# Optimization experiments

Measured on AMD Instinct MI355X. Metric: run time of the kernel, lower is better.

The kernel has to match this reference:

```python
import jax, jax.numpy as jnp
import numpy as np
from jax import lax

L, D, V, T = 12, 1024, 50277, 1024
F4 = 4 * D


def setup_inputs() -> dict:
    key = jax.random.key(0)
    ks = jax.random.split(key, 20)
    s = 0.02  # weight scale keeps k (exp argument) well-conditioned
    n = lambda k, shape, scale=s: jax.random.normal(k, shape, dtype=jnp.float32) * scale
    u = lambda k, shape: jax.random.uniform(k, shape, dtype=jnp.float32)
    return {
        "tokens": jax.random.randint(ks[0], (T,), 0, V, dtype=jnp.int32),
        "emb": n(ks[1], (V, D), 1.0),
        "ln0_w": jnp.ones((D,), jnp.float32), "ln0_b": jnp.zeros((D,), jnp.float32),
        "ln1_w": jnp.ones((L, D), jnp.float32), "ln1_b": jnp.zeros((L, D), jnp.float32),
        "ln2_w": jnp.ones((L, D), jnp.float32), "ln2_b": jnp.zeros((L, D), jnp.float32),
        "tmk": u(ks[2], (L, D)), "tmv": u(ks[3], (L, D)), "tmr": u(ks[4], (L, D)),
        "tmk_ffn": u(ks[5], (L, D)), "tmr_ffn": u(ks[6], (L, D)),
        "time_first": n(ks[7], (L, D), 0.5),
        "time_decay": -jnp.exp(n(ks[8], (L, D), 0.5)),  # __init__: -exp(raw)
        "att_kw": n(ks[9], (L, D, D)), "att_vw": n(ks[10], (L, D, D)),
        "att_rw": n(ks[11], (L, D, D)), "att_ow": n(ks[12], (L, D, D)),
        "ffn_kw": n(ks[13], (L, D, F4)), "ffn_vw": n(ks[14], (L, F4, D)),
        "ffn_rw": n(ks[15], (L, D, D)),
        "lnout_w": jnp.ones((D,), jnp.float32), "lnout_b": jnp.zeros((D,), jnp.float32),
        "head": n(ks[16], (V, D)),
    }


def _ln(x, w, b):
    mu = jnp.mean(x, -1, keepdims=True)
    var = jnp.var(x, -1, keepdims=True)
    return (x - mu) / jnp.sqrt(var + 1e-5) * w + b


def _shift(x):  # token shift: prepend zero state row (state init is zeros)
    return jnp.concatenate([jnp.zeros_like(x[:1]), x[:-1]], axis=0)


def _wkv(k, v, tf, td):  # k,v: [T,D]; aa/bb/pp scan with running-max exp trick
    init = (jnp.zeros_like(k[0]), jnp.zeros_like(k[0]), jnp.full_like(k[0], -1e30))
    def step(c, kv):
        aa, bb, pp = c
        kt, vt = kv
        ww = tf + kt
        p = jnp.maximum(pp, ww)
        e1 = jnp.exp(pp - p); e2 = jnp.exp(ww - p)
        out = (e1 * aa + e2 * vt) / (e1 * bb + e2)
        ww2 = pp + td
        p2 = jnp.maximum(ww2, kt)
        e1 = jnp.exp(ww2 - p2); e2 = jnp.exp(kt - p2)
        return (e1 * aa + e2 * vt, e1 * bb + e2, p2), out
    _, out = lax.scan(step, init, (k, v))
    return out


def reference(tokens, emb, ln0_w, ln0_b, ln1_w, ln1_b, ln2_w, ln2_b, tmk, tmv, tmr,
              tmk_ffn, tmr_ffn, time_first, time_decay, att_kw, att_vw, att_rw, att_ow,
              ffn_kw, ffn_vw, ffn_rw, lnout_w, lnout_b, head):
    x = _ln(emb[tokens], ln0_w, ln0_b)  # [T,D]; ln0 applied to emb rows as in __init__
    for i in range(L):
        # time-mix (attention) block
        xn = _ln(x, ln1_w[i], ln1_b[i])
        xx = _shift(xn)
        xk = xn * tmk[i] + xx * (1 - tmk[i])
        xv = xn * tmv[i] + xx * (1 - tmv[i])
        xr = xn * tmr[i] + xx * (1 - tmr[i])
        r = jax.nn.sigmoid(xr @ att_rw[i])
        k = xk @ att_kw[i]
        v = xv @ att_vw[i]
        wkv = _wkv(k, v, time_first[i], time_decay[i])
        x = x + (r * wkv) @ att_ow[i]
        # channel-mix (ffn) block
        xn = _ln(x, ln2_w[i], ln2_b[i])
        xx = _shift(xn)
        xk = xn * tmk_ffn[i] + xx * (1 - tmk_ffn[i])
        xr = xn * tmr_ffn[i] + xx * (1 - tmr_ffn[i])
        rf = jax.nn.sigmoid(xr @ ffn_rw[i])
        kf = jnp.square(jax.nn.relu(xk @ ffn_kw[i]))
        x = x + rf * (kf @ ffn_vw[i])
    xo = _ln(x[-1], lnout_w, lnout_b)
    return head @ xo  # logits [V]
```

## Files before the change

### kernel.cpp

```cpp
#include <hip/hip_runtime.h>

#define Tn 1024
#define Dn 1024
#define Ln 12
#define F4n 4096
#define Vn 50277
#define TDn (Tn*Dn)
#define MEG 1048576
#define SEG 16
#define NSEG 64

typedef __attribute__((ext_vector_type(4))) float f4;
typedef __attribute__((ext_vector_type(16))) float f32x16;
typedef __attribute__((ext_vector_type(8))) short short8;
typedef unsigned short u16;
typedef unsigned int u32;
typedef __attribute__((ext_vector_type(4))) u16 us4;

#define ASG __attribute__((address_space(1)))
#define ASL __attribute__((address_space(3)))

__device__ __forceinline__ u16 f2b(float x){
  u32 u = __float_as_uint(x);
  return (u16)((u + 0x7fffu + ((u >> 16) & 1u)) >> 16);
}

__device__ __forceinline__ f4 blockReduce4(f4 v){
  __shared__ f4 s[4];
  int lane = threadIdx.x & 63, w = threadIdx.x >> 6;
#pragma unroll
  for(int o = 32; o; o >>= 1){
    v.x += __shfl_xor(v.x, o);
    v.y += __shfl_xor(v.y, o);
    v.z += __shfl_xor(v.z, o);
    v.w += __shfl_xor(v.w, o);
  }
  if(lane == 0) s[w] = v;
  __syncthreads();
  return s[0] + s[1] + s[2] + s[3];
}

struct ConvArgs {
  const float* s0; const float* s1; const float* s2; const float* s3;
  const float* skw;
  const float* svw;
  const float* srw;
  u16* dst;
};
__global__ __launch_bounds__(256) void conv_k(ConvArgs a){
  __shared__ __align__(16) u16 t[64][68];
  int b = blockIdx.x, tid = threadIdx.x;
  const float* src; u16* dst; int K, N, tk, tn;
  if(b < 1024){
    int m = b >> 8, bt = b & 255;
    src = (m==0)?a.s0:((m==1)?a.s1:((m==2)?a.s2:a.s3));
    dst = a.dst + (size_t)m*MEG; K=1024; N=1024; tk=bt>>4; tn=bt&15;
  } else if(b < 2048){
    int bt = b-1024; src=a.skw; dst=a.dst+(size_t)4*MEG; K=1024; N=4096; tk=bt>>6; tn=bt&63;
  } else if(b < 3072){
    int bt = b-2048; src=a.svw; dst=a.dst+(size_t)8*MEG; K=4096; N=1024; tk=bt>>4; tn=bt&15;
  } else {
    int bt = b-3072; src=a.srw; dst=a.dst+(size_t)12*MEG; K=1024; N=1024; tk=bt>>4; tn=bt&15;
  }
  int rr0 = tid >> 4, c4 = (tid & 15)*4;
#pragma unroll
  for(int p=0;p<4;p++){
    int r = p*16 + rr0;
    f4 v = *(const f4*)(src + (size_t)(tk*64+r)*N + tn*64 + c4);
    us4 h; h[0]=f2b(v.x); h[1]=f2b(v.y); h[2]=f2b(v.z); h[3]=f2b(v.w);
    *(us4*)&t[r][c4] = h;
  }
  __syncthreads();
  int q = tid & 3, n = tid >> 2;
  int k0 = q*16;
  union { short8 v; u16 h[8]; } o0, o1;
#pragma unroll
  for(int j=0;j<8;j++){ o0.h[j]=t[k0+j][n]; o1.h[j]=t[k0+8+j][n]; }
  u16* dp = dst + (size_t)(tn*64+n)*K + tk*64 + k0;
  *(short8*)dp       = o0.v;
  *(short8*)(dp + 8) = o1.v;
}

__global__ __launch_bounds__(256) void embed_ln0_k(
    const int* __restrict__ tok, const float* __restrict__ emb,
    const float* __restrict__ w, const float* __restrict__ b,
    float* __restrict__ x){
  int t = blockIdx.x, tid = threadIdx.x;
  const f4* src = (const f4*)(emb + (size_t)tok[t] * Dn);
  f4 v = src[tid];
  f4 st;
  st.x = v.x+v.y+v.z+v.w;
  st.y = v.x*v.x+v.y*v.y+v.z*v.z+v.w*v.w;
  st.z = 0.f; st.w = 0.f;
  f4 red = blockReduce4(st);
  float mu = red.x * (1.0f/Dn);
  float rs = rsqrtf(red.y * (1.0f/Dn) - mu*mu + 1e-5f);
  f4 wv = ((const f4*)w)[tid], bv = ((const f4*)b)[tid];
  f4 o;
  o.x = (v.x-mu)*rs*wv.x + bv.x;
  o.y = (v.y-mu)*rs*wv.y + bv.y;
  o.z = (v.z-mu)*rs*wv.z + bv.z;
  o.w = (v.w-mu)*rs*wv.w + bv.w;
  ((f4*)(x + (size_t)t*Dn))[tid] = o;
}

__global__ __launch_bounds__(256) void ln_mix_att_k(
    const float* __restrict__ x,
    const float* __restrict__ lw, const float* __restrict__ lb,
    const float* __restrict__ tk, const float* __restrict__ tv, const float* __restrict__ tr,
    u16* __restrict__ xkvr){
  int t = blockIdx.x, tid = threadIdx.x;
  f4 cur = ((const f4*)(x + (size_t)t*Dn))[tid];
  f4 prv; prv.x=0.f; prv.y=0.f; prv.z=0.f; prv.w=0.f;
  if(t > 0) prv = ((const f4*)(x + (size_t)(t-1)*Dn))[tid];
  f4 st;
  st.x = cur.x+cur.y+cur.z+cur.w;
  st.y = cur.x*cur.x+cur.y*cur.y+cur.z*cur.z+cur.w*cur.w;
  st.z = prv.x+prv.y+prv.z+prv.w;
  st.w = prv.x*prv.x+prv.y*prv.y+prv.z*prv.z+prv.w*prv.w;
  f4 red = blockReduce4(st);
  float muc = red.x*(1.f/Dn), rsc = rsqrtf(red.y*(1.f/Dn)-muc*muc+1e-5f);
  float mup = red.z*(1.f/Dn), rsp = rsqrtf(red.w*(1.f/Dn)-mup*mup+1e-5f);
  f4 wv=((const f4*)lw)[tid], bv=((const f4*)lb)[tid];
  f4 kv=((const f4*)tk)[tid], vv=((const f4*)tv)[tid], rv=((const f4*)tr)[tid];
  us4 ok, ov, orr;
  float xn, xp;
#define MIX3(j, cj, pj, wj, bj, kj, vj, rj) \
  xn = (cj - muc)*rsc*wj + bj; \
  xp = (t>0) ? ((pj - mup)*rsp*wj + bj) : 0.f; \
  ok[j]  = f2b(xn*kj + xp*(1.f-kj)); \
  ov[j]  = f2b(xn*vj + xp*(1.f-vj)); \
  orr[j] = f2b(xn*rj + xp*(1.f-rj));
  MIX3(0, cur.x, prv.x, wv.x, bv.x, kv.x, vv.x, rv.x)
  MIX3(1, cur.y, prv.y, wv.y, bv.y, kv.y, vv.y, rv.y)
  MIX3(2, cur.z, prv.z, wv.z, bv.z, kv.z, vv.z, rv.z)
  MIX3(3, cur.w, prv.w, wv.w, bv.w, kv.w, vv.w, rv.w)
#undef MIX3
  size_t o0 = (size_t)t*Dn + tid*4;
  *(us4*)(xkvr + o0)         = ok;
  *(us4*)(xkvr + TDn + o0)   = ov;
  *(us4*)(xkvr + 2*TDn + o0) = orr;
}

__global__ __launch_bounds__(256) void ln_mix_ffn_k(
    const float* __restrict__ x,
    const float* __restrict__ lw, const float* __restrict__ lb,
    const float* __restrict__ tk, const float* __restrict__ tr,
    u16* __restrict__ xkr){
  int t = blockIdx.x, tid = threadIdx.x;
  f4 cur = ((const f4*)(x + (size_t)t*Dn))[tid];
  f4 prv; prv.x=0.f; prv.y=0.f; prv.z=0.f; prv.w=0.f;
  if(t > 0) prv = ((const f4*)(x + (size_t)(t-1)*Dn))[tid];
  f4 st;
  st.x = cur.x+cur.y+cur.z+cur.w;
  st.y = cur.x*cur.x+cur.y*cur.y+cur.z*cur.z+cur.w*cur.w;
  st.z = prv.x+prv.y+prv.z+prv.w;
  st.w = prv.x*prv.x+prv.y*prv.y+prv.z*prv.z+prv.w*prv.w;
  f4 red = blockReduce4(st);
  float muc = red.x*(1.f/Dn), rsc = rsqrtf(red.y*(1.f/Dn)-muc*muc+1e-5f);
  float mup = red.z*(1.f/Dn), rsp = rsqrtf(red.w*(1.f/Dn)-mup*mup+1e-5f);
  f4 wv=((const f4*)lw)[tid], bv=((const f4*)lb)[tid];
  f4 kv=((const f4*)tk)[tid], rv=((const f4*)tr)[tid];
  us4 ok, orr;
  float xn, xp;
#define MIX2(j, cj, pj, wj, bj, kj, rj) \
  xn = (cj - muc)*rsc*wj + bj; \
  xp = (t>0) ? ((pj - mup)*rsp*wj + bj) : 0.f; \
  ok[j]  = f2b(xn*kj + xp*(1.f-kj)); \
  orr[j] = f2b(xn*rj + xp*(1.f-rj));
  MIX2(0, cur.x, prv.x, wv.x, bv.x, kv.x, rv.x)
  MIX2(1, cur.y, prv.y, wv.y, bv.y, kv.y, rv.y)
  MIX2(2, cur.z, prv.z, wv.z, bv.z, kv.z, rv.z)
  MIX2(3, cur.w, prv.w, wv.w, bv.w, kv.w, rv.w)
#undef MIX2
  size_t o0 = (size_t)t*Dn + tid*4;
  *(us4*)(xkr + o0)       = ok;
  *(us4*)(xkr + TDn + o0) = orr;
}

__global__ __launch_bounds__(256) void wkv_seg_k(
    const float* __restrict__ kb, const float* __restrict__ vb,
    const float* __restrict__ tdp,
    float* __restrict__ sega, float* __restrict__ segb, float* __restrict__ segp){
  int ch = blockIdx.x*256 + threadIdx.x;
  int g = blockIdx.y;
  int t0 = g*SEG;
  float td = tdp[ch];
  float kk[SEG], vv[SEG];
#pragma unroll
  for(int j=0;j<SEG;j++){
    kk[j] = kb[(size_t)(t0+j)*Dn + ch];
    vv[j] = vb[(size_t)(t0+j)*Dn + ch];
  }
  float aa=0.f, bb=0.f, pp=-1e30f;
#pragma unroll
  for(int j=0;j<SEG;j++){
    float ww2 = pp + td;
    float p2 = fmaxf(ww2, kk[j]);
    float e1 = __expf(ww2-p2), e2 = __expf(kk[j]-p2);
    aa = e1*aa + e2*vv[j]; bb = e1*bb + e2; pp = p2;
  }
  size_t o = (size_t)g*Dn + ch;
  sega[o] = aa; segb[o] = bb; segp[o] = pp;
}

__global__ __launch_bounds__(256) void wkv_scan_k(
    const float* __restrict__ sega, const float* __restrict__ segb, const float* __restrict__ segp,
    const float* __restrict__ tdp,
    float* __restrict__ prea, float* __restrict__ preb, float* __restrict__ prep){
  int ch = blockIdx.x*256 + threadIdx.x;
  float Std = tdp[ch] * (float)SEG;
  float a=0.f, b=0.f, p=-1e30f;
  for(int g=0; g<NSEG; g++){
    size_t o = (size_t)g*Dn + ch;
    prea[o]=a; preb[o]=b; prep[o]=p;
    float ag=sega[o], bg=segb[o], qg=segp[o];
    float psh = p + Std;
    float pn = fmaxf(psh, qg);
    float eo = __expf(psh-pn), en = __expf(qg-pn);
    a = eo*a + en*ag; b = eo*b + en*bg; p = pn;
  }
}

__global__ __launch_bounds__(256) void wkv_out_k(
    const float* __restrict__ kb, const float* __restrict__ vb, const float* __restrict__ rb,
    const float* __restrict__ tfp, const float* __restrict__ tdp,
    const float* __restrict__ prea, const float* __restrict__ preb, const float* __restrict__ prep,
    u16* __restrict__ att_in){
  int ch = blockIdx.x*256 + threadIdx.x;
  int g = blockIdx.y;
  int t0 = g*SEG;
  float tf = tfp[ch], td = tdp[ch];
  size_t so = (size_t)g*Dn + ch;
  float aa = prea[so], bb = preb[so], pp = prep[so];
  float kk[SEG], vv[SEG], rr[SEG];
#pragma unroll
  for(int j=0;j<SEG;j++){
    kk[j]=kb[(size_t)(t0+j)*Dn+ch];
    vv[j]=vb[(size_t)(t0+j)*Dn+ch];
    rr[j]=rb[(size_t)(t0+j)*Dn+ch];
  }
#pragma unroll
  for(int j=0;j<SEG;j++){
    float kt=kk[j], vt=vv[j];
    float ww = tf + kt;
    float p = fmaxf(pp, ww);
    float e1 = __expf(pp-p), e2 = __expf(ww-p);
    float out = __fdividef(e1*aa+e2*vt, e1*bb+e2);
    float sig = __fdividef(1.f, 1.f+__expf(-rr[j]));
    att_in[(size_t)(t0+j)*Dn+ch] = f2b(sig*out);
    float ww2 = pp+td;
    float p2 = fmaxf(ww2,kt);
    e1 = __expf(ww2-p2); e2 = __expf(kt-p2);
    aa = e1*aa+e2*vt; bb = e1*bb+e2; pp = p2;
  }
}

template<int EPI, int KSTEP>
__global__ __launch_bounds__(128) void gemm_k(
    const u16* __restrict__ A, size_t ldA, size_t strideA,
    const u16* __restrict__ Bt, size_t ldB, size_t strideB,
    int K, int N,
    float* __restrict__ Cf, size_t strideC, u16* __restrict__ Cb,
    const float* __restrict__ aux){
  extern __shared__ __align__(16) u16 ldsd[];
  constexpr int RPC = 512/KSTEP;
  constexpr int LPR = 64/RPC;
  constexpr int NQ  = 32/RPC;
  constexpr int NS  = KSTEP/32;
  const int tid = threadIdx.x;
  const int l = tid & 63, w = tid >> 6;
  const int z = blockIdx.z;
  const int row0 = blockIdx.y*64, col0 = blockIdx.x*64;

  const u16* bA = A  + (size_t)z*strideA + (size_t)row0*ldA;
  const u16* bB = Bt + (size_t)z*strideB + (size_t)col0*ldB;

  int offA[NQ], offB[NQ], ldso[NQ];
#pragma unroll
  for(int q=0;q<NQ;q++){
    int ch = q*2 + w;
    int r  = ch*RPC + l/LPR;
    int phys = (l%LPR)*16;
    int kk = ((phys ^ ((r&15)<<4)) >> 1);
    offA[q] = r*(int)ldA + kk;
    offB[q] = r*(int)ldB + kk;
    ldso[q] = ch*512;
  }
  int foff[2][NS];
#pragma unroll
  for(int i=0;i<2;i++){
    int row = i*32 + (l&31);
#pragma unroll
    for(int s=0;s<NS;s++){
      int c = w*KSTEP + s*32 + ((l>>5)*16);
      foff[i][s] = row*KSTEP + ((c ^ ((row&15)<<4)) >> 1);
    }
  }

  f32x16 acc[2][2];
#pragma unroll
  for(int i=0;i<2;i++)
#pragma unroll
    for(int j=0;j<2;j++)
#pragma unroll
      for(int e=0;e<16;e++) acc[i][j][e] = 0.f;

  u16* ldsA0 = ldsd;
  u16* ldsB0 = ldsd + 64*KSTEP;
  u16* ldsA1 = ldsd + 2*64*KSTEP;
  u16* ldsB1 = ldsd + 3*64*KSTEP;

#define STAGE(LA, LB) do{ \
  _Pragma("unroll") \
  for(int q=0;q<NQ;q++){ \
    __builtin_amdgcn_global_load_lds((ASG const void*)(const void*)(bA + offA[q]), (ASL void*)(void*)((LA) + ldso[q]), 16, 0, 0); \
    __builtin_amdgcn_global_load_lds((ASG const void*)(const void*)(bB + offB[q]), (ASL void*)(void*)((LB) + ldso[q]), 16, 0, 0); \
  } \
  bA += KSTEP; bB += KSTEP; }while(0)

  const int nss = K / KSTEP;
  STAGE(ldsA0, ldsB0);
  __syncthreads();
  int buf = 0;
  for(int ss=0; ss<nss; ss++){
    if(ss+1 < nss){
      if(buf) STAGE(ldsA0, ldsB0); else STAGE(ldsA1, ldsB1);
    }
    const u16* La = buf ? ldsA1 : ldsA0;
    const u16* Lb = buf ? ldsB1 : ldsB0;
#pragma unroll
    for(int s=0;s<NS;s++){
      short8 a0 = *(const short8*)(La + foff[0][s]);
      short8 a1 = *(const short8*)(La + foff[1][s]);
      short8 b0 = *(const short8*)(Lb + foff[0][s]);
      short8 b1 = *(const short8*)(Lb + foff[1][s]);
      acc[0][0] = __builtin_amdgcn_mfma_f32_32x32x16_bf16(a0, b0, acc[0][0], 0, 0, 0);
      acc[0][1] = __builtin_amdgcn_mfma_f32_32x32x16_bf16(a0, b1, acc[0][1], 0, 0, 0);
      acc[1][0] = __builtin_amdgcn_mfma_f32_32x32x16_bf16(a1, b0, acc[1][0], 0, 0, 0);
      acc[1][1] = __builtin_amdgcn_mfma_f32_32x32x16_bf16(a1, b1, acc[1][1], 0, 0, 0);
    }
    __syncthreads();
    buf ^= 1;
  }
#undef STAGE

  float* red = (float*)ldsd;
  if(w == 1){
#pragma unroll
    for(int i=0;i<2;i++)
#pragma unroll
      for(int j=0;j<2;j++)
#pragma unroll
        for(int reg=0;reg<16;reg++){
          int rr_ = (reg&3) + 8*(reg>>2) + 4*(l>>5);
          red[(size_t)(i*32 + rr_)*64 + j*32 + (l&31)] = acc[i][j][reg];
        }
  }
  __syncthreads();
  if(w == 0){
#pragma unroll
    for(int i=0;i<2;i++)
#pragma unroll
      for(int j=0;j<2;j++)
#pragma unroll
        for(int reg=0;reg<16;reg++){
          int rr_ = (reg&3) + 8*(reg>>2) + 4*(l>>5);
          float v = acc[i][j][reg] + red[(size_t)(i*32 + rr_)*64 + j*32 + (l&31)];
          int grow = row0 + i*32 + rr_;
          int gcol = col0 + j*32 + (l&31);
          size_t idx = (size_t)grow*N + gcol;
          if constexpr(EPI==0){ Cf[(size_t)z*strideC + idx] = v; }
          else if constexpr(EPI==1){ float t_ = v>0.f ? v : 0.f; Cb[idx] = f2b(t_*t_); }
          else if constexpr(EPI==2){ Cf[idx] += v; }
          else { float s_ = __fdividef(1.f, 1.f+__expf(-aux[idx])); Cf[idx] += s_*v; }
        }
  }
}

__global__ __launch_bounds__(256) void lnout_k(
    const float* __restrict__ x, const float* __restrict__ w, const float* __restrict__ b,
    float* __restrict__ xo){
  int tid = threadIdx.x;
  f4 v = ((const f4*)(x + (size_t)(Tn-1)*Dn))[tid];
  f4 st;
  st.x = v.x+v.y+v.z+v.w;
  st.y = v.x*v.x+v.y*v.y+v.z*v.z+v.w*v.w;
  st.z = 0.f; st.w = 0.f;
  f4 red = blockReduce4(st);
  float mu = red.x*(1.f/Dn);
  float rs = rsqrtf(red.y*(1.f/Dn) - mu*mu + 1e-5f);
  f4 wv = ((const f4*)w)[tid], bv = ((const f4*)b)[tid];
  f4 o;
  o.x = (v.x-mu)*rs*wv.x + bv.x;
  o.y = (v.y-mu)*rs*wv.y + bv.y;
  o.z = (v.z-mu)*rs*wv.z + bv.z;
  o.w = (v.w-mu)*rs*wv.w + bv.w;
  ((f4*)xo)[tid] = o;
}

__global__ __launch_bounds__(256) void head_k(
    const float* __restrict__ head, const float* __restrict__ xo, float* __restrict__ out){
  __shared__ f4 sxo[256];
  int tid = threadIdx.x;
  sxo[tid] = ((const f4*)xo)[tid];
  __syncthreads();
  int w = tid >> 6, lane = tid & 63;
  int row = blockIdx.x*4 + w;
  if(row < Vn){
    const f4* hr = (const f4*)(head + (size_t)row*Dn);
    float s = 0.f;
#pragma unroll
    for(int i=0;i<4;i++){
      f4 h = hr[i*64 + lane];
      f4 xv = sxo[i*64 + lane];
      s += h.x*xv.x + h.y*xv.y + h.z*xv.z + h.w*xv.w;
    }
#pragma unroll
    for(int o=32;o;o>>=1) s += __shfl_xor(s, o);
    if(lane == 0) out[row] = s;
  }
}

extern "C" void kernel_launch(void* const* d_in, const int* in_sizes, int n_in,
                              void* d_out, int out_size, void* d_ws, size_t ws_size,
                              hipStream_t stream) {
  (void)in_sizes; (void)n_in; (void)out_size; (void)ws_size;
  const int*   tokens   = (const int*)  d_in[0];
  const float* emb      = (const float*)d_in[1];
  const float* ln0_w    = (const float*)d_in[2];
  const float* ln0_b    = (const float*)d_in[3];
  const float* ln1_w    = (const float*)d_in[4];
  const float* ln1_b    = (const float*)d_in[5];
  const float* ln2_w    = (const float*)d_in[6];
  const float* ln2_b    = (const float*)d_in[7];
  const float* tmk      = (const float*)d_in[8];
  const float* tmv      = (const float*)d_in[9];
  const float* tmr      = (const float*)d_in[10];
  const float* tmk_ffn  = (const float*)d_in[11];
  const float* tmr_ffn  = (const float*)d_in[12];
  const float* tfirst   = (const float*)d_in[13];
  const float* tdecay   = (const float*)d_in[14];
  const float* att_kw   = (const float*)d_in[15];
  const float* att_vw   = (const float*)d_in[16];
  const float* att_rw   = (const float*)d_in[17];
  const float* att_ow   = (const float*)d_in[18];
  const float* ffn_kw   = (const float*)d_in[19];
  const float* ffn_vw   = (const float*)d_in[20];
  const float* ffn_rw   = (const float*)d_in[21];
  const float* lnoutw   = (const float*)d_in[22];
  const float* lnoutb   = (const float*)d_in[23];
  const float* headw    = (const float*)d_in[24];
  float* logits = (float*)d_out;

  char* wsb = (char*)d_ws;
  size_t off = 0;
  auto carve = [&](size_t bytes)->void*{
    void* p = wsb + off;
    off += (bytes + 255) & ~(size_t)255;
    return p;
  };
  float* x      = (float*)carve((size_t)TDn*4);
  u16*   xkvr   = (u16*)  carve((size_t)3*TDn*2);
  float* kvr    = (float*)carve((size_t)3*TDn*4);
  u16*   att_in = (u16*)  carve((size_t)TDn*2);
  u16*   xkr    = (u16*)  carve((size_t)2*TDn*2);
  u16*   kf     = (u16*)  carve((size_t)Tn*F4n*2);
  float* rf     = (float*)carve((size_t)TDn*4);
  float* xo     = (float*)carve((size_t)Dn*4);
  u16*   wbt    = (u16*)  carve((size_t)13*MEG*2);
  float* sega   = (float*)carve((size_t)NSEG*Dn*4);
  float* segb   = (float*)carve((size_t)NSEG*Dn*4);
  float* segp   = (float*)carve((size_t)NSEG*Dn*4);
  float* prea   = (float*)carve((size_t)NSEG*Dn*4);
  float* preb   = (float*)carve((size_t)NSEG*Dn*4);
  float* prep   = (float*)carve((size_t)NSEG*Dn*4);

  embed_ln0_k<<<Tn, 256, 0, stream>>>(tokens, emb, ln0_w, ln0_b, x);

  for(int i=0;i<Ln;i++){
    size_t dd = (size_t)i*Dn*Dn;
    ConvArgs ca;
    ca.s0 = att_kw+dd; ca.s1 = att_vw+dd; ca.s2 = att_rw+dd; ca.s3 = att_ow+dd;
    ca.skw = ffn_kw+(size_t)i*Dn*F4n; ca.svw = ffn_vw+(size_t)i*F4n*Dn; ca.srw = ffn_rw+dd;
    ca.dst = wbt;
    conv_k<<<3328, 256, 0, stream>>>(ca);

    ln_mix_att_k<<<Tn, 256, 0, stream>>>(x, ln1_w+i*Dn, ln1_b+i*Dn,
                                         tmk+i*Dn, tmv+i*Dn, tmr+i*Dn, xkvr);
    gemm_k<0,128><<<dim3(16,16,3), 128, 65536, stream>>>(
        xkvr, Dn, (size_t)TDn, wbt, Dn, (size_t)MEG, Dn, Dn,
        kvr, (size_t)TDn, nullptr, nullptr);
    wkv_seg_k<<<dim3(4,NSEG), 256, 0, stream>>>(kvr, kvr+TDn, tdecay+i*Dn, sega, segb, segp);
    wkv_scan_k<<<4, 256, 0, stream>>>(sega, segb, segp, tdecay+i*Dn, prea, preb, prep);
    wkv_out_k<<<dim3(4,NSEG), 256, 0, stream>>>(kvr, kvr+TDn, kvr+2*TDn,
                                                tfirst+i*Dn, tdecay+i*Dn,
                                                prea, preb, prep, att_in);
    gemm_k<2,256><<<dim3(16,16,1), 128, 131072, stream>>>(
        att_in, Dn, 0, wbt+(size_t)3*MEG, Dn, 0, Dn, Dn,
        x, 0, nullptr, nullptr);
    ln_mix_ffn_k<<<Tn, 256, 0, stream>>>(x, ln2_w+i*Dn, ln2_b+i*Dn,
                                         tmk_ffn+i*Dn, tmr_ffn+i*Dn, xkr);
    gemm_k<1,128><<<dim3(64,16,1), 128, 65536, stream>>>(
        xkr, Dn, 0, wbt+(size_t)4*MEG, Dn, 0, Dn, F4n,
        nullptr, 0, kf, nullptr);
    gemm_k<0,256><<<dim3(16,16,1), 128, 131072, stream>>>(
        xkr+TDn, Dn, 0, wbt+(size_t)12*MEG, Dn, 0, Dn, Dn,
        rf, 0, nullptr, nullptr);
    gemm_k<3,256><<<dim3(16,16,1), 128, 131072, stream>>>(
        kf, F4n, 0, wbt+(size_t)8*MEG, F4n, 0, F4n, Dn,
        x, 0, nullptr, rf);
  }

  lnout_k<<<1, 256, 0, stream>>>(x, lnoutw, lnoutb, xo);
  head_k<<<(Vn+3)/4, 256, 0, stream>>>(headw, xo, logits);
}
```

Baseline: 1.906 ms.

## Fuse WKV segment-prefix scan into output kernel and merge FFN key/receptance GEMMs

Drops the separate single-pass WKV prefix-scan kernel. Each output block now recomputes its own segment prefix by folding the preceding segment summaries, which removes one launch and the prefix buffers but adds redundant quadratic work over segments. The FFN key GEMM and the receptance GEMM become one grid-launched kernel with a dedicated double-buffered LDS pipeline, so the smaller GEMM fills leftover CUs and one launch is saved. The cost is a new hand-written GEMM path with a fixed 64x64 tile and a branch on block index for the epilogue.

```diff
diff --git a/kernel.cpp b/kernel.cpp
--- a/kernel.cpp
+++ b/kernel.cpp
@@ -204,35 +204,25 @@
   sega[o] = aa; segb[o] = bb; segp[o] = pp;
 }
 
-__global__ __launch_bounds__(256) void wkv_scan_k(
-    const float* __restrict__ sega, const float* __restrict__ segb, const float* __restrict__ segp,
-    const float* __restrict__ tdp,
-    float* __restrict__ prea, float* __restrict__ preb, float* __restrict__ prep){
-  int ch = blockIdx.x*256 + threadIdx.x;
-  float Std = tdp[ch] * (float)SEG;
-  float a=0.f, b=0.f, p=-1e30f;
-  for(int g=0; g<NSEG; g++){
-    size_t o = (size_t)g*Dn + ch;
-    prea[o]=a; preb[o]=b; prep[o]=p;
-    float ag=sega[o], bg=segb[o], qg=segp[o];
-    float psh = p + Std;
-    float pn = fmaxf(psh, qg);
-    float eo = __expf(psh-pn), en = __expf(qg-pn);
-    a = eo*a + en*ag; b = eo*b + en*bg; p = pn;
-  }
-}
-
-__global__ __launch_bounds__(256) void wkv_out_k(
+__global__ __launch_bounds__(256) void wkv_outscan_k(
     const float* __restrict__ kb, const float* __restrict__ vb, const float* __restrict__ rb,
     const float* __restrict__ tfp, const float* __restrict__ tdp,
-    const float* __restrict__ prea, const float* __restrict__ preb, const float* __restrict__ prep,
+    const float* __restrict__ sega, const float* __restrict__ segb, const float* __restrict__ segp,
     u16* __restrict__ att_in){
   int ch = blockIdx.x*256 + threadIdx.x;
   int g = blockIdx.y;
   int t0 = g*SEG;
   float tf = tfp[ch], td = tdp[ch];
-  size_t so = (size_t)g*Dn + ch;
-  float aa = prea[so], bb = preb[so], pp = prep[so];
+  float Std = td * (float)SEG;
+  float aa=0.f, bb=0.f, pp=-1e30f;
+  for(int j=0;j<g;j++){
+    size_t o = (size_t)j*Dn + ch;
+    float ag=sega[o], bg=segb[o], qg=segp[o];
+    float psh = pp + Std;
+    float pn = fmaxf(psh, qg);
+    float eo = __expf(psh-pn), en = __expf(qg-pn);
+    aa = eo*aa + en*ag; bb = eo*bb + en*bg; pp = pn;
+  }
   float kk[SEG], vv[SEG], rr[SEG];
 #pragma unroll
   for(int j=0;j<SEG;j++){
@@ -374,6 +364,112 @@
           else if constexpr(EPI==1){ float t_ = v>0.f ? v : 0.f; Cb[idx] = f2b(t_*t_); }
           else if constexpr(EPI==2){ Cf[idx] += v; }
           else { float s_ = __fdividef(1.f, 1.f+__expf(-aux[idx])); Cf[idx] += s_*v; }
+        }
+  }
+}
+
+__global__ __launch_bounds__(128) void gemm_fkr_k(
+    const u16* __restrict__ xkr, const u16* __restrict__ wl,
+    u16* __restrict__ kf, float* __restrict__ rf){
+  __shared__ __align__(16) u16 lds[2][2][64*128];
+  const int tid = threadIdx.x;
+  const int l = tid & 63, w = tid >> 6;
+  const bool isfk = blockIdx.x < 64;
+  const u16* Az = isfk ? xkr : xkr + TDn;
+  const u16* Bz = isfk ? wl + (size_t)4*MEG : wl + (size_t)12*MEG;
+  const int N = isfk ? F4n : Dn;
+  const int col0 = (isfk ? blockIdx.x : blockIdx.x-64)*64;
+  const int row0 = blockIdx.y*64;
+
+  const u16* pA[8]; const u16* pB[8]; int ldsoff[8];
+#pragma unroll
+  for(int q=0;q<8;q++){
+    int r = (q*2+w)*4 + (l>>4);
+    int kk = (((l&15)*16) ^ ((r&15)<<4)) >> 1;
+    pA[q] = Az + (size_t)(row0+r)*Dn + kk;
+    pB[q] = Bz + (size_t)(col0+r)*Dn + kk;
+    ldsoff[q] = (q*2+w)*512;
+  }
+  int foff[2][4];
+#pragma unroll
+  for(int i=0;i<2;i++){
+    int row = i*32 + (l&31);
+#pragma unroll
+    for(int s=0;s<4;s++){
+      int c = w*128 + s*32 + ((l>>5)*16);
+      foff[i][s] = row*128 + ((c ^ ((row&15)<<4)) >> 1);
+    }
+  }
+
+  f32x16 acc[2][2];
+#pragma unroll
+  for(int i=0;i<2;i++)
+#pragma unroll
+    for(int j=0;j<2;j++)
+#pragma unroll
+      for(int e=0;e<16;e++) acc[i][j][e] = 0.f;
+
+#define STAGE(BUF) do{ \
+  _Pragma("unroll") \
+  for(int q=0;q<8;q++){ \
+    __builtin_amdgcn_global_load_lds((ASG const void*)(const void*)pA[q], (ASL void*)(void*)&lds[BUF][0][ldsoff[q]], 16, 0, 0); \
+    __builtin_amdgcn_global_load_lds((ASG const void*)(const void*)pB[q], (ASL void*)(void*)&lds[BUF][1][ldsoff[q]], 16, 0, 0); \
+    pA[q] += 128; pB[q] += 128; \
+  } }while(0)
+
+  STAGE(0);
+  __syncthreads();
+  int buf = 0;
+#pragma unroll 1
+  for(int ss=0; ss<8; ss++){
+    if(ss+1 < 8){
+      if(buf) STAGE(0); else STAGE(1);
+    }
+    const u16* La = &lds[buf][0][0];
+    const u16* Lb = &lds[buf][1][0];
+#pragma unroll
+    for(int s=0;s<4;s++){
+      short8 a0 = *(const short8*)(La + foff[0][s]);
+      short8 a1 = *(const short8*)(La + foff[1][s]);
+      short8 b0 = *(const short8*)(Lb + foff[0][s]);
+      short8 b1 = *(const short8*)(Lb + foff[1][s]);
+      acc[0][0] = __builtin_amdgcn_mfma_f32_32x32x16_bf16(a0, b0, acc[0][0], 0, 0, 0);
+      acc[0][1] = __builtin_amdgcn_mfma_f32_32x32x16_bf16(a0, b1, acc[0][1], 0, 0, 0);
+      acc[1][0] = __builtin_amdgcn_mfma_f32_32x32x16_bf16(a1, b0, acc[1][0], 0, 0, 0);
+      acc[1][1] = __builtin_amdgcn_mfma_f32_32x32x16_bf16(a1, b1, acc[1][1], 0, 0, 0);
+    }
+    __syncthreads();
+    buf ^= 1;
+  }
+#undef STAGE
+
+  float* red = (float*)&lds[0][0][0];
+  if(w == 1){
+#pragma unroll
+    for(int i=0;i<2;i++)
+#pragma unroll
+      for(int j=0;j<2;j++)
+#pragma unroll
+        for(int reg=0;reg<16;reg++){
+          int rr_ = (reg&3) + 8*(reg>>2) + 4*(l>>5);
+          red[(size_t)(i*32 + rr_)*64 + j*32 + (l&31)] = acc[i][j][reg];
+        }
+  }
+  __syncthreads();
+  if(w == 0){
+#pragma unroll
+    for(int i=0;i<2;i++)
+#pragma unroll
+      for(int j=0;j<2;j++)
+#pragma unroll
+        for(int reg=0;reg<16;reg++){
+          int rr_ = (reg&3) + 8*(reg>>2) + 4*(l>>5);
+          float v = acc[i][j][reg] + red[(size_t)(i*32 + rr_)*64 + j*32 + (l&31)];
+          int grow = row0 + i*32 + rr_;
+          int gcol = col0 + j*32 + (l&31);
+          size_t idx = (size_t)grow*N + gcol;
+          if(isfk){ float t_ = v>0.f ? v : 0.f; kf[idx] = f2b(t_*t_); }
+          else rf[idx] = v;
         }
   }
 }
@@ -472,9 +568,6 @@
   float* sega   = (float*)carve((size_t)NSEG*Dn*4);
   float* segb   = (float*)carve((size_t)NSEG*Dn*4);
   float* segp   = (float*)carve((size_t)NSEG*Dn*4);
-  float* prea   = (float*)carve((size_t)NSEG*Dn*4);
-  float* preb   = (float*)carve((size_t)NSEG*Dn*4);
-  float* prep   = (float*)carve((size_t)NSEG*Dn*4);
 
   embed_ln0_k<<<Tn, 256, 0, stream>>>(tokens, emb, ln0_w, ln0_b, x);
 
@@ -492,21 +585,15 @@
         xkvr, Dn, (size_t)TDn, wbt, Dn, (size_t)MEG, Dn, Dn,
         kvr, (size_t)TDn, nullptr, nullptr);
     wkv_seg_k<<<dim3(4,NSEG), 256, 0, stream>>>(kvr, kvr+TDn, tdecay+i*Dn, sega, segb, segp);
-    wkv_scan_k<<<4, 256, 0, stream>>>(sega, segb, segp, tdecay+i*Dn, prea, preb, prep);
-    wkv_out_k<<<dim3(4,NSEG), 256, 0, stream>>>(kvr, kvr+TDn, kvr+2*TDn,
-                                                tfirst+i*Dn, tdecay+i*Dn,
-                                                prea, preb, prep, att_in);
+    wkv_outscan_k<<<dim3(4,NSEG), 256, 0, stream>>>(kvr, kvr+TDn, kvr+2*TDn,
+                                                    tfirst+i*Dn, tdecay+i*Dn,
+                                                    sega, segb, segp, att_in);
     gemm_k<2,256><<<dim3(16,16,1), 128, 131072, stream>>>(
         att_in, Dn, 0, wbt+(size_t)3*MEG, Dn, 0, Dn, Dn,
         x, 0, nullptr, nullptr);
     ln_mix_ffn_k<<<Tn, 256, 0, stream>>>(x, ln2_w+i*Dn, ln2_b+i*Dn,
                                          tmk_ffn+i*Dn, tmr_ffn+i*Dn, xkr);
-    gemm_k<1,128><<<dim3(64,16,1), 128, 65536, stream>>>(
-        xkr, Dn, 0, wbt+(size_t)4*MEG, Dn, 0, Dn, F4n,
-        nullptr, 0, kf, nullptr);
-    gemm_k<0,256><<<dim3(16,16,1), 128, 131072, stream>>>(
-        xkr+TDn, Dn, 0, wbt+(size_t)12*MEG, Dn, 0, Dn, Dn,
-        rf, 0, nullptr, nullptr);
+    gemm_fkr_k<<<dim3(80,16), 128, 0, stream>>>(xkr, wbt, kf, rf);
     gemm_k<3,256><<<dim3(16,16,1), 128, 131072, stream>>>(
         kf, F4n, 0, wbt+(size_t)8*MEG, F4n, 0, F4n, Dn,
         x, 0, nullptr, rf);
```

Result: slower. 2.031 ms (+6.5%).

## Fuse WKV segment, scan and output kernels into one cooperative kernel

Applied to the files above, without the earlier changes.

Replaces the three WKV kernels (segment reduce, cross-segment scan, output) with a single cooperative launch of 512 blocks of 128 threads that uses grid.sync between phases. The aim is to remove two kernel launches and their inter-kernel gaps per layer. In exchange, grid-wide barriers are added, and during the scan phase only 8 blocks do work while the rest wait. The cooperative launch also carries its own fixed overhead.

```diff
diff --git a/kernel.cpp b/kernel.cpp
--- a/kernel.cpp
+++ b/kernel.cpp
@@ -1,4 +1,7 @@
 #include <hip/hip_runtime.h>
+#include <hip/hip_cooperative_groups.h>
+
+namespace cg = cooperative_groups;
 
 #define Tn 1024
 #define Dn 1024
@@ -178,81 +181,82 @@
   *(us4*)(xkr + TDn + o0) = orr;
 }
 
-__global__ __launch_bounds__(256) void wkv_seg_k(
-    const float* __restrict__ kb, const float* __restrict__ vb,
-    const float* __restrict__ tdp,
-    float* __restrict__ sega, float* __restrict__ segb, float* __restrict__ segp){
-  int ch = blockIdx.x*256 + threadIdx.x;
-  int g = blockIdx.y;
-  int t0 = g*SEG;
-  float td = tdp[ch];
-  float kk[SEG], vv[SEG];
-#pragma unroll
-  for(int j=0;j<SEG;j++){
-    kk[j] = kb[(size_t)(t0+j)*Dn + ch];
-    vv[j] = vb[(size_t)(t0+j)*Dn + ch];
-  }
-  float aa=0.f, bb=0.f, pp=-1e30f;
-#pragma unroll
-  for(int j=0;j<SEG;j++){
-    float ww2 = pp + td;
-    float p2 = fmaxf(ww2, kk[j]);
-    float e1 = __expf(ww2-p2), e2 = __expf(kk[j]-p2);
-    aa = e1*aa + e2*vv[j]; bb = e1*bb + e2; pp = p2;
-  }
-  size_t o = (size_t)g*Dn + ch;
-  sega[o] = aa; segb[o] = bb; segp[o] = pp;
-}
-
-__global__ __launch_bounds__(256) void wkv_scan_k(
-    const float* __restrict__ sega, const float* __restrict__ segb, const float* __restrict__ segp,
-    const float* __restrict__ tdp,
-    float* __restrict__ prea, float* __restrict__ preb, float* __restrict__ prep){
-  int ch = blockIdx.x*256 + threadIdx.x;
-  float Std = tdp[ch] * (float)SEG;
-  float a=0.f, b=0.f, p=-1e30f;
-  for(int g=0; g<NSEG; g++){
-    size_t o = (size_t)g*Dn + ch;
-    prea[o]=a; preb[o]=b; prep[o]=p;
-    float ag=sega[o], bg=segb[o], qg=segp[o];
-    float psh = p + Std;
-    float pn = fmaxf(psh, qg);
-    float eo = __expf(psh-pn), en = __expf(qg-pn);
-    a = eo*a + en*ag; b = eo*b + en*bg; p = pn;
-  }
-}
-
-__global__ __launch_bounds__(256) void wkv_out_k(
+__global__ __launch_bounds__(128) void wkv_coop_k(
     const float* __restrict__ kb, const float* __restrict__ vb, const float* __restrict__ rb,
     const float* __restrict__ tfp, const float* __restrict__ tdp,
-    const float* __restrict__ prea, const float* __restrict__ preb, const float* __restrict__ prep,
+    float* __restrict__ sega, float* __restrict__ segb, float* __restrict__ segp,
+    float* __restrict__ prea, float* __restrict__ preb, float* __restrict__ prep,
     u16* __restrict__ att_in){
-  int ch = blockIdx.x*256 + threadIdx.x;
-  int g = blockIdx.y;
-  int t0 = g*SEG;
-  float tf = tfp[ch], td = tdp[ch];
-  size_t so = (size_t)g*Dn + ch;
-  float aa = prea[so], bb = preb[so], pp = prep[so];
-  float kk[SEG], vv[SEG], rr[SEG];
-#pragma unroll
-  for(int j=0;j<SEG;j++){
-    kk[j]=kb[(size_t)(t0+j)*Dn+ch];
-    vv[j]=vb[(size_t)(t0+j)*Dn+ch];
-    rr[j]=rb[(size_t)(t0+j)*Dn+ch];
-  }
-#pragma unroll
-  for(int j=0;j<SEG;j++){
-    float kt=kk[j], vt=vv[j];
-    float ww = tf + kt;
-    float p = fmaxf(pp, ww);
-    float e1 = __expf(pp-p), e2 = __expf(ww-p);
-    float out = __fdividef(e1*aa+e2*vt, e1*bb+e2);
-    float sig = __fdividef(1.f, 1.f+__expf(-rr[j]));
-    att_in[(size_t)(t0+j)*Dn+ch] = f2b(sig*out);
-    float ww2 = pp+td;
-    float p2 = fmaxf(ww2,kt);
-    e1 = __expf(ww2-p2); e2 = __expf(kt-p2);
-    aa = e1*aa+e2*vt; bb = e1*bb+e2; pp = p2;
+  cg::grid_group grid = cg::this_grid();
+  const int b = blockIdx.x, tid = threadIdx.x;
+  const int c = b & 7, g = b >> 3;
+  const int ch = c*128 + tid;
+  const int t0 = g*SEG;
+  const float td = tdp[ch];
+
+  {
+    float kk[SEG], vv[SEG];
+#pragma unroll
+    for(int j=0;j<SEG;j++){
+      kk[j] = kb[(size_t)(t0+j)*Dn + ch];
+      vv[j] = vb[(size_t)(t0+j)*Dn + ch];
+    }
+    float aa=0.f, bb=0.f, pp=-1e30f;
+#pragma unroll
+    for(int j=0;j<SEG;j++){
+      float ww2 = pp + td;
+      float p2 = fmaxf(ww2, kk[j]);
+      float e1 = __expf(ww2-p2), e2 = __expf(kk[j]-p2);
+      aa = e1*aa + e2*vv[j]; bb = e1*bb + e2; pp = p2;
+    }
+    size_t o = (size_t)g*Dn + ch;
+    sega[o] = aa; segb[o] = bb; segp[o] = pp;
+  }
+  __threadfence();
+  grid.sync();
+
+  if(b < 8){
+    int sch = b*128 + tid;
+    float Std = tdp[sch] * (float)SEG;
+    float a=0.f, bb2=0.f, p=-1e30f;
+    for(int gg=0; gg<NSEG; gg++){
+      size_t o = (size_t)gg*Dn + sch;
+      prea[o]=a; preb[o]=bb2; prep[o]=p;
+      float ag=sega[o], bg=segb[o], qg=segp[o];
+      float psh = p + Std;
+      float pn = fmaxf(psh, qg);
+      float eo = __expf(psh-pn), en = __expf(qg-pn);
+      a = eo*a + en*ag; bb2 = eo*bb2 + en*bg; p = pn;
+    }
+  }
+  __threadfence();
+  grid.sync();
+
+  {
+    const float tf = tfp[ch];
+    size_t so = (size_t)g*Dn + ch;
+    float aa = prea[so], bb = preb[so], pp = prep[so];
+    float kk[SEG], vv[SEG], rr[SEG];
+#pragma unroll
+    for(int j=0;j<SEG;j++){
+      kk[j]=kb[(size_t)(t0+j)*Dn+ch];
+      vv[j]=vb[(size_t)(t0+j)*Dn+ch];
+      rr[j]=rb[(size_t)(t0+j)*Dn+ch];
+    }
+#pragma unroll
+    for(int j=0;j<SEG;j++){
+      float kt=kk[j], vt=vv[j];
+      float ww = tf + kt;
+      float p = fmaxf(pp, ww);
+      float e1 = __expf(pp-p), e2 = __expf(ww-p);
+      float out = __fdividef(e1*aa+e2*vt, e1*bb+e2);
+      float sig = __fdividef(1.f, 1.f+__expf(-rr[j]));
+      att_in[(size_t)(t0+j)*Dn+ch] = f2b(sig*out);
+      float ww2 = pp+td;
+      float p2 = fmaxf(ww2,kt);
+      e1 = __expf(ww2-p2); e2 = __expf(kt-p2);
+      aa = e1*aa+e2*vt; bb = e1*bb+e2; pp = p2;
+    }
   }
 }
 
@@ -491,11 +495,20 @@
     gemm_k<0,128><<<dim3(16,16,3), 128, 65536, stream>>>(
         xkvr, Dn, (size_t)TDn, wbt, Dn, (size_t)MEG, Dn, Dn,
         kvr, (size_t)TDn, nullptr, nullptr);
-    wkv_seg_k<<<dim3(4,NSEG), 256, 0, stream>>>(kvr, kvr+TDn, tdecay+i*Dn, sega, segb, segp);
-    wkv_scan_k<<<4, 256, 0, stream>>>(sega, segb, segp, tdecay+i*Dn, prea, preb, prep);
-    wkv_out_k<<<dim3(4,NSEG), 256, 0, stream>>>(kvr, kvr+TDn, kvr+2*TDn,
-                                                tfirst+i*Dn, tdecay+i*Dn,
-                                                prea, preb, prep, att_in);
+    {
+      const float* kbp = kvr;
+      const float* vbp = kvr + TDn;
+      const float* rbp = kvr + 2*TDn;
+      const float* tfp = tfirst + i*Dn;
+      const float* tdp = tdecay + i*Dn;
+      void* cargs[] = { (void*)&kbp, (void*)&vbp, (void*)&rbp,
+                        (void*)&tfp, (void*)&tdp,
+                        (void*)&sega, (void*)&segb, (void*)&segp,
+                        (void*)&prea, (void*)&preb, (void*)&prep,
+                        (void*)&att_in };
+      hipLaunchCooperativeKernel((const void*)wkv_coop_k, dim3(512), dim3(128),
+                                 cargs, 0, stream);
+    }
     gemm_k<2,256><<<dim3(16,16,1), 128, 131072, stream>>>(
         att_in, Dn, 0, wbt+(size_t)3*MEG, Dn, 0, Dn, Dn,
         x, 0, nullptr, nullptr);
```

Result: slower. 3.463 ms (+81.7%).
